# Kernel optimization log

Hardware: AMD Instinct MI355X
Metric: run time of the kernel (lower is better)

Reference implementation:

```python
import jax, jax.numpy as jnp
import numpy as np

N = 4096      # nodes
F = 512       # input_dim
D = 512       # output_dim
H = 8         # n_heads
d = D // H    # per-head out_sz


def setup_inputs() -> dict:
    key = jax.random.key(0)
    ks = jax.random.split(key, 6)
    x = jax.random.normal(ks[0], (N, F), dtype=jnp.float32)
    adj = (jax.random.uniform(ks[1], (N, N)) < 0.01).astype(jnp.float32)
    adj = jnp.maximum(adj, jnp.eye(N, dtype=jnp.float32))
    # per-head params: weight transform W, attention vectors a1/a2 (conv1d k=1 -> dot) with biases
    W = jax.random.normal(ks[2], (H, F, d), dtype=jnp.float32) * 0.05
    a1 = jax.random.normal(ks[3], (H, d), dtype=jnp.float32) * 0.05
    a2 = jax.random.normal(ks[4], (H, d), dtype=jnp.float32) * 0.05
    b1 = jnp.zeros((H,), dtype=jnp.float32)
    b2 = jnp.zeros((H,), dtype=jnp.float32)
    return {"x": x, "adj": adj, "W": W, "a1": a1, "b1": b1, "a2": a2, "b2": b2}


def reference(x, adj, W, a1, b1, a2, b2):
    # per-node linear transform for all heads: [H, N, d]
    seq_fts = jnp.einsum('nf,hfd->hnd', x, W)
    # attention logits components (conv1d(out=1,k=1) == dot + bias): [H, N]
    f1 = jnp.einsum('hnd,hd->hn', seq_fts, a1) + b1[:, None]
    f2 = jnp.einsum('hnd,hd->hn', seq_fts, a2) + b2[:, None]
    # logits = adj * f1_i + adj * f2_j  (adj acts multiplicatively AND as sparsity mask)
    logits = adj[None, :, :] * f1[:, :, None] + adj[None, :, :] * f2[:, None, :]
    lrelu = jnp.maximum(0.2 * logits, logits)  # leaky_relu alpha=0.2
    # sparse softmax over adjacency nonzeros (tf.sparse_softmax over from_dense pattern)
    mask = adj != 0
    scores = jnp.where(mask[None, :, :], lrelu, -jnp.inf)
    coefs = jax.nn.softmax(scores, axis=-1)           # [H, N, N], zero off-mask
    vals = jnp.einsum('hnm,hmd->hnd', coefs, seq_fts)  # sparse-dense matmul per head
    # concat heads on feature axis, batch dim of 1, elu activation
    h = jnp.transpose(vals, (1, 0, 2)).reshape(N, H * d)[None, :, :]
    return jax.nn.elu(h)
```

## Files before the change

### kernel.cpp

```cpp
#include <hip/hip_runtime.h>
#include <math.h>

#define N_NODES 4096
#define F_DIM   512
#define D_DIM   512
#define H_HEADS 8
#define HD      64
#define CAP     128

typedef __attribute__((ext_vector_type(8))) short short8;
typedef __attribute__((ext_vector_type(4))) float f32x4;

__device__ __forceinline__ unsigned short f2bf(float f) {
    unsigned int u = __builtin_bit_cast(unsigned int, f);
    return (unsigned short)((u + 0x7FFFu + ((u >> 16) & 1u)) >> 16);
}
__device__ __forceinline__ float bflo(unsigned int u) {
    return __builtin_bit_cast(float, u << 16);
}
__device__ __forceinline__ float bfhi(unsigned int u) {
    return __builtin_bit_cast(float, u & 0xffff0000u);
}

__global__ __launch_bounds__(256) void conv_w(const float* __restrict__ W,
                                              unsigned short* __restrict__ Bt) {
    const int t = blockIdx.x * 256 + threadIdx.x;
    const int n = t >> 6;
    const int kb = (t & 63) * 8;
    const int h = n >> 6, dd = n & 63;
    const float* src = W + (size_t)h * F_DIM * HD + dd;
    unsigned short o[8];
    #pragma unroll
    for (int q = 0; q < 8; ++q) o[q] = f2bf(src[(size_t)(kb + q) * HD]);
    *(uint4*)&Bt[(size_t)n * F_DIM + kb] = *(const uint4*)o;
}

__global__ __launch_bounds__(256) void mega(const float* __restrict__ x,
                                            const unsigned short* __restrict__ Bt,
                                            const float* __restrict__ adj,
                                            const float* __restrict__ a1,
                                            const float* __restrict__ b1,
                                            const float* __restrict__ a2,
                                            const float* __restrict__ b2,
                                            unsigned short* __restrict__ seqb,
                                            float* __restrict__ f1t,
                                            float* __restrict__ f2t,
                                            unsigned short* __restrict__ rowIdx,
                                            int* __restrict__ cntArr) {
    __shared__ unsigned short As[64][40];
    __shared__ unsigned short Bs[64][40];
    __shared__ float sF[2][64][2];

    const int tid  = threadIdx.x;
    const int lane = tid & 63;
    const int w    = tid >> 6;

    if (blockIdx.x >= 512) {
        const int r = (blockIdx.x - 512) * 4 + w;
        const float* arow = adj + (size_t)r * N_NODES;

        f32x4 vq[16];
        #pragma unroll
        for (int q = 0; q < 16; ++q)
            vq[q] = *(const f32x4*)&arow[q * 256 + lane * 4];

        unsigned long long mask = 0ull;
        #pragma unroll
        for (int q = 0; q < 16; ++q) {
            if (vq[q].x != 0.0f) mask |= 1ull << (q * 4 + 0);
            if (vq[q].y != 0.0f) mask |= 1ull << (q * 4 + 1);
            if (vq[q].z != 0.0f) mask |= 1ull << (q * 4 + 2);
            if (vq[q].w != 0.0f) mask |= 1ull << (q * 4 + 3);
        }
        const int n_t = __popcll(mask);
        int incl = n_t;
        #pragma unroll
        for (int off = 1; off < 64; off <<= 1) {
            int u = __shfl_up(incl, off, 64);
            if (lane >= off) incl += u;
        }
        const int tot = __shfl(incl, 63, 64);
        int pos = incl - n_t;
        unsigned short* rbase = rowIdx + (size_t)r * CAP;
        while (mask) {
            const int bit = __builtin_ctzll(mask);
            mask &= mask - 1;
            const int col = ((bit >> 2) << 8) + (lane << 2) + (bit & 3);
            if (pos < CAP)
                __builtin_nontemporal_store((unsigned short)col, rbase + pos);
            ++pos;
        }
        if (lane == 0) cntArr[r] = tot;
        return;
    }

    const int wr   = w >> 1, wc = w & 1;
    const int i0   = (blockIdx.x & 63) * 64;
    const int h    = blockIdx.x >> 6;
    const int n0   = h * 64;

    const int ar = tid >> 2;
    const int ac = (tid & 3) * 8;

    const int rlane = lane & 15;
    const int q     = lane >> 4;
    const int klane = q * 8;

    f32x4 acc[2][2] = {};

    for (int k0 = 0; k0 < F_DIM; k0 += 32) {
        const float* ga = &x[(size_t)(i0 + ar) * F_DIM + k0 + ac];
        const float4 xa = *(const float4*)ga;
        const float4 xb4 = *(const float4*)(ga + 4);
        unsigned short ao[8] = {f2bf(xa.x), f2bf(xa.y), f2bf(xa.z), f2bf(xa.w),
                                f2bf(xb4.x), f2bf(xb4.y), f2bf(xb4.z), f2bf(xb4.w)};
        const uint4 bv = *(const uint4*)&Bt[(size_t)(n0 + ar) * F_DIM + k0 + ac];
        __syncthreads();
        *(uint4*)&As[ar][ac] = *(const uint4*)ao;
        *(uint4*)&Bs[ar][ac] = bv;
        __syncthreads();

        short8 a_frag[2], b_frag[2];
        #pragma unroll
        for (int mi = 0; mi < 2; ++mi)
            a_frag[mi] = *(const short8*)&As[wr * 32 + mi * 16 + rlane][klane];
        #pragma unroll
        for (int ni = 0; ni < 2; ++ni)
            b_frag[ni] = *(const short8*)&Bs[wc * 32 + ni * 16 + rlane][klane];
        #pragma unroll
        for (int mi = 0; mi < 2; ++mi)
            #pragma unroll
            for (int ni = 0; ni < 2; ++ni)
                acc[mi][ni] = __builtin_amdgcn_mfma_f32_16x16x32_bf16(
                    a_frag[mi], b_frag[ni], acc[mi][ni], 0, 0, 0);
    }

    #pragma unroll
    for (int mi = 0; mi < 2; ++mi)
        #pragma unroll
        for (int ni = 0; ni < 2; ++ni)
            #pragma unroll
            for (int r = 0; r < 4; ++r) {
                const int row = i0 + wr * 32 + mi * 16 + q * 4 + r;
                const int col = n0 + wc * 32 + ni * 16 + rlane;
                seqb[(size_t)row * D_DIM + col] = f2bf(acc[mi][ni][r]);
            }

    float a1v[2], a2v[2];
    #pragma unroll
    for (int ni = 0; ni < 2; ++ni) {
        const int c = wc * 32 + ni * 16 + rlane;
        a1v[ni] = a1[h * HD + c];
        a2v[ni] = a2[h * HD + c];
    }
    #pragma unroll
    for (int mi = 0; mi < 2; ++mi)
        #pragma unroll
        for (int r = 0; r < 4; ++r) {
            float s1 = acc[mi][0][r] * a1v[0] + acc[mi][1][r] * a1v[1];
            float s2 = acc[mi][0][r] * a2v[0] + acc[mi][1][r] * a2v[1];
            #pragma unroll
            for (int m = 1; m < 16; m <<= 1) {
                s1 += __shfl_xor(s1, m, 64);
                s2 += __shfl_xor(s2, m, 64);
            }
            if (rlane == 0) {
                const int rl = wr * 32 + mi * 16 + q * 4 + r;
                sF[0][rl][wc] = s1;
                sF[1][rl][wc] = s2;
            }
        }
    __syncthreads();
    if (tid < 64) {
        const int row = i0 + tid;
        f1t[row * 8 + h] = sF[0][tid][0] + sF[0][tid][1] + b1[h];
        f2t[row * 8 + h] = sF[1][tid][0] + sF[1][tid][1] + b2[h];
    }
}

__global__ __launch_bounds__(128) void attn(const float* __restrict__ adj,
                                            const unsigned short* __restrict__ seqb,
                                            const float* __restrict__ f1t,
                                            const float* __restrict__ f2t,
                                            const unsigned short* __restrict__ rowIdx,
                                            const int* __restrict__ cntArr,
                                            float* __restrict__ out) {
    __shared__ int   sIdx[CAP];
    __shared__ float sP[CAP][8];
    __shared__ float sRedS[2][8];
    __shared__ float sAcc[64][8];

    const int i    = blockIdx.x;
    const int tid  = threadIdx.x;
    const int lane = tid & 63;
    const int w    = tid >> 6;
    const int h8   = lane >> 3;

    const int cnt = cntArr[i];

    const float4 f1a = *(const float4*)&f1t[i * 8];
    const float4 f1b = *(const float4*)&f1t[i * 8 + 4];
    const float f1r[8] = {f1a.x, f1a.y, f1a.z, f1a.w, f1b.x, f1b.y, f1b.z, f1b.w};

    float accv[8] = {0.f, 0.f, 0.f, 0.f, 0.f, 0.f, 0.f, 0.f};
    float myinv;

    if (cnt <= CAP) {
        int j = 0;
        float s[8] = {0.f, 0.f, 0.f, 0.f, 0.f, 0.f, 0.f, 0.f};
        float e[8] = {0.f, 0.f, 0.f, 0.f, 0.f, 0.f, 0.f, 0.f};
        if (tid < cnt) {
            j = (int)__builtin_nontemporal_load(rowIdx + (size_t)i * CAP + tid);
            const float4 fa = *(const float4*)&f2t[j * 8];
            const float4 fb = *(const float4*)&f2t[j * 8 + 4];
            const float f2r[8] = {fa.x, fa.y, fa.z, fa.w, fb.x, fb.y, fb.z, fb.w};
            #pragma unroll
            for (int h = 0; h < 8; ++h) {
                float v = f1r[h] + f2r[h];
                v = fmaxf(v, 0.2f * v);
                e[h] = __expf(v);
                s[h] = e[h];
            }
        }
        sIdx[tid] = j;
        f32x4 ea = {e[0], e[1], e[2], e[3]};
        f32x4 eb = {e[4], e[5], e[6], e[7]};
        *(f32x4*)&sP[tid][0] = ea;
        *(f32x4*)&sP[tid][4] = eb;

        #pragma unroll
        for (int off = 32; off; off >>= 1)
            #pragma unroll
            for (int h = 0; h < 8; ++h)
                s[h] += __shfl_xor(s[h], off, 64);
        if (lane == 0) {
            f32x4 sa = {s[0], s[1], s[2], s[3]};
            f32x4 sb = {s[4], s[5], s[6], s[7]};
            *(f32x4*)&sRedS[w][0] = sa;
            *(f32x4*)&sRedS[w][4] = sb;
        }
        __syncthreads();
        myinv = 1.0f / (sRedS[0][h8] + sRedS[1][h8]);

        const int G = (cnt + 3) >> 2;
        const char* __restrict__ vbase = (const char*)seqb + lane * 16;
        int g = w;
        if (g < G) {
            int4 jC = *(const int4*)&sIdx[g * 4];
            float pC0 = sP[g * 4 + 0][h8];
            float pC1 = sP[g * 4 + 1][h8];
            float pC2 = sP[g * 4 + 2][h8];
            float pC3 = sP[g * 4 + 3][h8];
            uint4 u0 = *(const uint4*)(vbase + ((size_t)jC.x << 10));
            uint4 u1 = *(const uint4*)(vbase + ((size_t)jC.y << 10));
            uint4 u2 = *(const uint4*)(vbase + ((size_t)jC.z << 10));
            uint4 u3 = *(const uint4*)(vbase + ((size_t)jC.w << 10));
            for (;;) {
                const int gn = g + 2;
                const bool more = gn < G;
                int4 jN;
                float pN0, pN1, pN2, pN3;
                uint4 v0, v1, v2, v3;
                if (more) {
                    jN = *(const int4*)&sIdx[gn * 4];
                    pN0 = sP[gn * 4 + 0][h8];
                    pN1 = sP[gn * 4 + 1][h8];
                    pN2 = sP[gn * 4 + 2][h8];
                    pN3 = sP[gn * 4 + 3][h8];
                    v0 = *(const uint4*)(vbase + ((size_t)jN.x << 10));
                    v1 = *(const uint4*)(vbase + ((size_t)jN.y << 10));
                    v2 = *(const uint4*)(vbase + ((size_t)jN.z << 10));
                    v3 = *(const uint4*)(vbase + ((size_t)jN.w << 10));
                }
                const unsigned int w0[4] = {u0.x, u0.y, u0.z, u0.w};
                const unsigned int w1[4] = {u1.x, u1.y, u1.z, u1.w};
                const unsigned int w2[4] = {u2.x, u2.y, u2.z, u2.w};
                const unsigned int w3[4] = {u3.x, u3.y, u3.z, u3.w};
                #pragma unroll
                for (int k = 0; k < 4; ++k) {
                    accv[k * 2 + 0] = fmaf(pC0, bflo(w0[k]), accv[k * 2 + 0]);
                    accv[k * 2 + 1] = fmaf(pC0, bfhi(w0[k]), accv[k * 2 + 1]);
                    accv[k * 2 + 0] = fmaf(pC1, bflo(w1[k]), accv[k * 2 + 0]);
                    accv[k * 2 + 1] = fmaf(pC1, bfhi(w1[k]), accv[k * 2 + 1]);
                    accv[k * 2 + 0] = fmaf(pC2, bflo(w2[k]), accv[k * 2 + 0]);
                    accv[k * 2 + 1] = fmaf(pC2, bfhi(w2[k]), accv[k * 2 + 1]);
                    accv[k * 2 + 0] = fmaf(pC3, bflo(w3[k]), accv[k * 2 + 0]);
                    accv[k * 2 + 1] = fmaf(pC3, bfhi(w3[k]), accv[k * 2 + 1]);
                }
                if (!more) break;
                u0 = v0; u1 = v1; u2 = v2; u3 = v3;
                pC0 = pN0; pC1 = pN1; pC2 = pN2; pC3 = pN3;
                g = gn;
            }
        }
    } else {
        const float* arow = adj + (size_t)i * N_NODES;
        float s[8] = {0.f, 0.f, 0.f, 0.f, 0.f, 0.f, 0.f, 0.f};
        for (int jx = tid; jx < N_NODES; jx += 128) {
            if (arow[jx] != 0.0f) {
                const float4 fa = *(const float4*)&f2t[jx * 8];
                const float4 fb = *(const float4*)&f2t[jx * 8 + 4];
                const float f2r[8] = {fa.x, fa.y, fa.z, fa.w, fb.x, fb.y, fb.z, fb.w};
                #pragma unroll
                for (int h = 0; h < 8; ++h) {
                    float v = f1r[h] + f2r[h];
                    v = fmaxf(v, 0.2f * v);
                    s[h] += __expf(v);
                }
            }
        }
        #pragma unroll
        for (int off = 32; off; off >>= 1)
            #pragma unroll
            for (int h = 0; h < 8; ++h)
                s[h] += __shfl_xor(s[h], off, 64);
        if (lane == 0) {
            f32x4 sa = {s[0], s[1], s[2], s[3]};
            f32x4 sb = {s[4], s[5], s[6], s[7]};
            *(f32x4*)&sRedS[w][0] = sa;
            *(f32x4*)&sRedS[w][4] = sb;
        }
        __syncthreads();
        myinv = 1.0f / (sRedS[0][h8] + sRedS[1][h8]);
        const float f1h = f1r[h8];

        const char* __restrict__ vbase = (const char*)seqb + lane * 16;
        const int jlo = w * (N_NODES / 2), jhi = jlo + N_NODES / 2;
        for (int jx = jlo; jx < jhi; ++jx) {
            if (arow[jx] != 0.0f) {
                float v = f1h + f2t[jx * 8 + h8];
                v = fmaxf(v, 0.2f * v);
                const float p = __expf(v);
                const uint4 u = *(const uint4*)(vbase + ((size_t)jx << 10));
                const unsigned int wv[4] = {u.x, u.y, u.z, u.w};
                #pragma unroll
                for (int k = 0; k < 4; ++k) {
                    accv[k * 2 + 0] = fmaf(p, bflo(wv[k]), accv[k * 2 + 0]);
                    accv[k * 2 + 1] = fmaf(p, bfhi(wv[k]), accv[k * 2 + 1]);
                }
            }
        }
    }

    if (w == 1) {
        f32x4 pa = {accv[0], accv[1], accv[2], accv[3]};
        f32x4 pb = {accv[4], accv[5], accv[6], accv[7]};
        *(f32x4*)&sAcc[lane][0] = pa;
        *(f32x4*)&sAcc[lane][4] = pb;
    }
    __syncthreads();
    if (w == 0) {
        float o[8];
        #pragma unroll
        for (int k = 0; k < 8; ++k) {
            const float v = (accv[k] + sAcc[lane][k]) * myinv;
            o[k] = (v > 0.f) ? v : expm1f(v);
        }
        f32x4 oa = {o[0], o[1], o[2], o[3]};
        f32x4 ob = {o[4], o[5], o[6], o[7]};
        float* dst = &out[(size_t)i * D_DIM + lane * 8];
        __builtin_nontemporal_store(oa, (f32x4*)dst);
        __builtin_nontemporal_store(ob, (f32x4*)(dst + 4));
    }
}

extern "C" void kernel_launch(void* const* d_in, const int* in_sizes, int n_in,
                              void* d_out, int out_size, void* d_ws, size_t ws_size,
                              hipStream_t stream) {
    const float* x   = (const float*)d_in[0];
    const float* adj = (const float*)d_in[1];
    const float* W   = (const float*)d_in[2];
    const float* a1  = (const float*)d_in[3];
    const float* b1  = (const float*)d_in[4];
    const float* a2  = (const float*)d_in[5];
    const float* b2  = (const float*)d_in[6];
    float* out = (float*)d_out;

    char* ws = (char*)d_ws;
    unsigned short* seqb = (unsigned short*)ws;
    unsigned short* Bt   = (unsigned short*)(ws + (size_t)N_NODES * D_DIM * 2);
    float* f1t = (float*)(ws + (size_t)N_NODES * D_DIM * 2 + (size_t)D_DIM * F_DIM * 2);
    float* f2t = f1t + (size_t)N_NODES * H_HEADS;
    unsigned short* rowIdx = (unsigned short*)(f2t + (size_t)N_NODES * H_HEADS);
    int* cntArr = (int*)(rowIdx + (size_t)N_NODES * CAP);

    conv_w<<<128, 256, 0, stream>>>(W, Bt);

    mega<<<1536, 256, 0, stream>>>(x, Bt, adj, a1, b1, a2, b2,
                                   seqb, f1t, f2t, rowIdx, cntArr);

    attn<<<N_NODES, 128, 0, stream>>>(adj, seqb, f1t, f2t, rowIdx, cntArr, out);
}
```

Baseline: 43.95 us.

## Split attention aggregation per row into two single-wave blocks by head half

The attention kernel now launches two 64-thread blocks per node, each handling four heads (half of the feature columns), instead of one 128-thread block that split neighbours across two waves. This removes the cross-wave softmax-sum and accumulator reductions through shared memory, so one wave keeps the whole softmax row. The trade-off is that each block recomputes the exp scores for its half, gathered loads shrink to 8 bytes per lane, and the software prefetch of the next neighbour group is gone.

```diff
diff --git a/kernel.cpp b/kernel.cpp
--- a/kernel.cpp
+++ b/kernel.cpp
@@ -178,131 +178,118 @@
     }
 }
 
-__global__ __launch_bounds__(128) void attn(const float* __restrict__ adj,
-                                            const unsigned short* __restrict__ seqb,
-                                            const float* __restrict__ f1t,
-                                            const float* __restrict__ f2t,
-                                            const unsigned short* __restrict__ rowIdx,
-                                            const int* __restrict__ cntArr,
-                                            float* __restrict__ out) {
+__global__ __launch_bounds__(64) void attn(const float* __restrict__ adj,
+                                           const unsigned short* __restrict__ seqb,
+                                           const float* __restrict__ f1t,
+                                           const float* __restrict__ f2t,
+                                           const unsigned short* __restrict__ rowIdx,
+                                           const int* __restrict__ cntArr,
+                                           float* __restrict__ out) {
     __shared__ int   sIdx[CAP];
-    __shared__ float sP[CAP][8];
-    __shared__ float sRedS[2][8];
-    __shared__ float sAcc[64][8];
-
-    const int i    = blockIdx.x;
-    const int tid  = threadIdx.x;
-    const int lane = tid & 63;
-    const int w    = tid >> 6;
-    const int h8   = lane >> 3;
+    __shared__ float sP[CAP][4];
+
+    const int bid  = blockIdx.x;
+    const int half = bid >> 12;
+    const int i    = bid & (N_NODES - 1);
+    const int lane = threadIdx.x;
+    const int hq   = lane >> 4;
 
     const int cnt = cntArr[i];
 
-    const float4 f1a = *(const float4*)&f1t[i * 8];
-    const float4 f1b = *(const float4*)&f1t[i * 8 + 4];
-    const float f1r[8] = {f1a.x, f1a.y, f1a.z, f1a.w, f1b.x, f1b.y, f1b.z, f1b.w};
-
-    float accv[8] = {0.f, 0.f, 0.f, 0.f, 0.f, 0.f, 0.f, 0.f};
+    const float4 f1h4 = *(const float4*)&f1t[i * 8 + half * 4];
+    const float f1r[4] = {f1h4.x, f1h4.y, f1h4.z, f1h4.w};
+
+    float accv[4] = {0.f, 0.f, 0.f, 0.f};
     float myinv;
 
     if (cnt <= CAP) {
-        int j = 0;
-        float s[8] = {0.f, 0.f, 0.f, 0.f, 0.f, 0.f, 0.f, 0.f};
-        float e[8] = {0.f, 0.f, 0.f, 0.f, 0.f, 0.f, 0.f, 0.f};
-        if (tid < cnt) {
-            j = (int)__builtin_nontemporal_load(rowIdx + (size_t)i * CAP + tid);
-            const float4 fa = *(const float4*)&f2t[j * 8];
-            const float4 fb = *(const float4*)&f2t[j * 8 + 4];
-            const float f2r[8] = {fa.x, fa.y, fa.z, fa.w, fb.x, fb.y, fb.z, fb.w};
-            #pragma unroll
-            for (int h = 0; h < 8; ++h) {
+        int j0 = 0, j1 = 0;
+        float e0[4] = {0.f, 0.f, 0.f, 0.f};
+        float e1[4] = {0.f, 0.f, 0.f, 0.f};
+        const bool has0 = lane < cnt;
+        const bool has1 = lane + 64 < cnt;
+        if (has0) {
+            j0 = (int)rowIdx[(size_t)i * CAP + lane];
+            const float4 fv = *(const float4*)&f2t[j0 * 8 + half * 4];
+            const float f2r[4] = {fv.x, fv.y, fv.z, fv.w};
+            #pragma unroll
+            for (int h = 0; h < 4; ++h) {
                 float v = f1r[h] + f2r[h];
                 v = fmaxf(v, 0.2f * v);
-                e[h] = __expf(v);
-                s[h] = e[h];
-            }
-        }
-        sIdx[tid] = j;
-        f32x4 ea = {e[0], e[1], e[2], e[3]};
-        f32x4 eb = {e[4], e[5], e[6], e[7]};
-        *(f32x4*)&sP[tid][0] = ea;
-        *(f32x4*)&sP[tid][4] = eb;
-
+                e0[h] = __expf(v);
+            }
+        }
+        if (has1) {
+            j1 = (int)rowIdx[(size_t)i * CAP + lane + 64];
+            const float4 fv = *(const float4*)&f2t[j1 * 8 + half * 4];
+            const float f2r[4] = {fv.x, fv.y, fv.z, fv.w};
+            #pragma unroll
+            for (int h = 0; h < 4; ++h) {
+                float v = f1r[h] + f2r[h];
+                v = fmaxf(v, 0.2f * v);
+                e1[h] = __expf(v);
+            }
+        }
+        sIdx[lane]      = j0;
+        sIdx[lane + 64] = j1;
+        f32x4 ea = {e0[0], e0[1], e0[2], e0[3]};
+        f32x4 eb = {e1[0], e1[1], e1[2], e1[3]};
+        *(f32x4*)&sP[lane][0]      = ea;
+        *(f32x4*)&sP[lane + 64][0] = eb;
+
+        float s[4];
+        #pragma unroll
+        for (int h = 0; h < 4; ++h) s[h] = e0[h] + e1[h];
         #pragma unroll
         for (int off = 32; off; off >>= 1)
             #pragma unroll
-            for (int h = 0; h < 8; ++h)
+            for (int h = 0; h < 4; ++h)
                 s[h] += __shfl_xor(s[h], off, 64);
-        if (lane == 0) {
-            f32x4 sa = {s[0], s[1], s[2], s[3]};
-            f32x4 sb = {s[4], s[5], s[6], s[7]};
-            *(f32x4*)&sRedS[w][0] = sa;
-            *(f32x4*)&sRedS[w][4] = sb;
-        }
+        myinv = 1.0f;
+        #pragma unroll
+        for (int h = 0; h < 4; ++h)
+            if (h == hq) myinv = 1.0f / s[h];
         __syncthreads();
-        myinv = 1.0f / (sRedS[0][h8] + sRedS[1][h8]);
-
+
+        const char* __restrict__ vbase =
+            (const char*)seqb + half * 512 + lane * 8;
         const int G = (cnt + 3) >> 2;
-        const char* __restrict__ vbase = (const char*)seqb + lane * 16;
-        int g = w;
-        if (g < G) {
-            int4 jC = *(const int4*)&sIdx[g * 4];
-            float pC0 = sP[g * 4 + 0][h8];
-            float pC1 = sP[g * 4 + 1][h8];
-            float pC2 = sP[g * 4 + 2][h8];
-            float pC3 = sP[g * 4 + 3][h8];
-            uint4 u0 = *(const uint4*)(vbase + ((size_t)jC.x << 10));
-            uint4 u1 = *(const uint4*)(vbase + ((size_t)jC.y << 10));
-            uint4 u2 = *(const uint4*)(vbase + ((size_t)jC.z << 10));
-            uint4 u3 = *(const uint4*)(vbase + ((size_t)jC.w << 10));
-            for (;;) {
-                const int gn = g + 2;
-                const bool more = gn < G;
-                int4 jN;
-                float pN0, pN1, pN2, pN3;
-                uint4 v0, v1, v2, v3;
-                if (more) {
-                    jN = *(const int4*)&sIdx[gn * 4];
-                    pN0 = sP[gn * 4 + 0][h8];
-                    pN1 = sP[gn * 4 + 1][h8];
-                    pN2 = sP[gn * 4 + 2][h8];
-                    pN3 = sP[gn * 4 + 3][h8];
-                    v0 = *(const uint4*)(vbase + ((size_t)jN.x << 10));
-                    v1 = *(const uint4*)(vbase + ((size_t)jN.y << 10));
-                    v2 = *(const uint4*)(vbase + ((size_t)jN.z << 10));
-                    v3 = *(const uint4*)(vbase + ((size_t)jN.w << 10));
-                }
-                const unsigned int w0[4] = {u0.x, u0.y, u0.z, u0.w};
-                const unsigned int w1[4] = {u1.x, u1.y, u1.z, u1.w};
-                const unsigned int w2[4] = {u2.x, u2.y, u2.z, u2.w};
-                const unsigned int w3[4] = {u3.x, u3.y, u3.z, u3.w};
-                #pragma unroll
-                for (int k = 0; k < 4; ++k) {
-                    accv[k * 2 + 0] = fmaf(pC0, bflo(w0[k]), accv[k * 2 + 0]);
-                    accv[k * 2 + 1] = fmaf(pC0, bfhi(w0[k]), accv[k * 2 + 1]);
-                    accv[k * 2 + 0] = fmaf(pC1, bflo(w1[k]), accv[k * 2 + 0]);
-                    accv[k * 2 + 1] = fmaf(pC1, bfhi(w1[k]), accv[k * 2 + 1]);
-                    accv[k * 2 + 0] = fmaf(pC2, bflo(w2[k]), accv[k * 2 + 0]);
-                    accv[k * 2 + 1] = fmaf(pC2, bfhi(w2[k]), accv[k * 2 + 1]);
-                    accv[k * 2 + 0] = fmaf(pC3, bflo(w3[k]), accv[k * 2 + 0]);
-                    accv[k * 2 + 1] = fmaf(pC3, bfhi(w3[k]), accv[k * 2 + 1]);
-                }
-                if (!more) break;
-                u0 = v0; u1 = v1; u2 = v2; u3 = v3;
-                pC0 = pN0; pC1 = pN1; pC2 = pN2; pC3 = pN3;
-                g = gn;
-            }
+        for (int g = 0; g < G; ++g) {
+            const int4  j4 = *(const int4*)&sIdx[g * 4];
+            const float p0 = sP[g * 4 + 0][hq];
+            const float p1 = sP[g * 4 + 1][hq];
+            const float p2 = sP[g * 4 + 2][hq];
+            const float p3 = sP[g * 4 + 3][hq];
+            const uint2 u0 = *(const uint2*)(vbase + ((size_t)j4.x << 10));
+            const uint2 u1 = *(const uint2*)(vbase + ((size_t)j4.y << 10));
+            const uint2 u2 = *(const uint2*)(vbase + ((size_t)j4.z << 10));
+            const uint2 u3 = *(const uint2*)(vbase + ((size_t)j4.w << 10));
+            accv[0] = fmaf(p0, bflo(u0.x), accv[0]);
+            accv[1] = fmaf(p0, bfhi(u0.x), accv[1]);
+            accv[2] = fmaf(p0, bflo(u0.y), accv[2]);
+            accv[3] = fmaf(p0, bfhi(u0.y), accv[3]);
+            accv[0] = fmaf(p1, bflo(u1.x), accv[0]);
+            accv[1] = fmaf(p1, bfhi(u1.x), accv[1]);
+            accv[2] = fmaf(p1, bflo(u1.y), accv[2]);
+            accv[3] = fmaf(p1, bfhi(u1.y), accv[3]);
+            accv[0] = fmaf(p2, bflo(u2.x), accv[0]);
+            accv[1] = fmaf(p2, bfhi(u2.x), accv[1]);
+            accv[2] = fmaf(p2, bflo(u2.y), accv[2]);
+            accv[3] = fmaf(p2, bfhi(u2.y), accv[3]);
+            accv[0] = fmaf(p3, bflo(u3.x), accv[0]);
+            accv[1] = fmaf(p3, bfhi(u3.x), accv[1]);
+            accv[2] = fmaf(p3, bflo(u3.y), accv[2]);
+            accv[3] = fmaf(p3, bfhi(u3.y), accv[3]);
         }
     } else {
         const float* arow = adj + (size_t)i * N_NODES;
-        float s[8] = {0.f, 0.f, 0.f, 0.f, 0.f, 0.f, 0.f, 0.f};
-        for (int jx = tid; jx < N_NODES; jx += 128) {
+        float s[4] = {0.f, 0.f, 0.f, 0.f};
+        for (int jx = lane; jx < N_NODES; jx += 64) {
             if (arow[jx] != 0.0f) {
-                const float4 fa = *(const float4*)&f2t[jx * 8];
-                const float4 fb = *(const float4*)&f2t[jx * 8 + 4];
-                const float f2r[8] = {fa.x, fa.y, fa.z, fa.w, fb.x, fb.y, fb.z, fb.w};
+                const float4 fv = *(const float4*)&f2t[jx * 8 + half * 4];
+                const float f2r[4] = {fv.x, fv.y, fv.z, fv.w};
                 #pragma unroll
-                for (int h = 0; h < 8; ++h) {
+                for (int h = 0; h < 4; ++h) {
                     float v = f1r[h] + f2r[h];
                     v = fmaxf(v, 0.2f * v);
                     s[h] += __expf(v);
@@ -312,56 +299,39 @@
         #pragma unroll
         for (int off = 32; off; off >>= 1)
             #pragma unroll
-            for (int h = 0; h < 8; ++h)
+            for (int h = 0; h < 4; ++h)
                 s[h] += __shfl_xor(s[h], off, 64);
-        if (lane == 0) {
-            f32x4 sa = {s[0], s[1], s[2], s[3]};
-            f32x4 sb = {s[4], s[5], s[6], s[7]};
-            *(f32x4*)&sRedS[w][0] = sa;
-            *(f32x4*)&sRedS[w][4] = sb;
-        }
-        __syncthreads();
-        myinv = 1.0f / (sRedS[0][h8] + sRedS[1][h8]);
-        const float f1h = f1r[h8];
-
-        const char* __restrict__ vbase = (const char*)seqb + lane * 16;
-        const int jlo = w * (N_NODES / 2), jhi = jlo + N_NODES / 2;
-        for (int jx = jlo; jx < jhi; ++jx) {
+        myinv = 1.0f;
+        #pragma unroll
+        for (int h = 0; h < 4; ++h)
+            if (h == hq) myinv = 1.0f / s[h];
+        const float f1h = f1r[hq];
+
+        const char* __restrict__ vbase =
+            (const char*)seqb + half * 512 + lane * 8;
+        for (int jx = 0; jx < N_NODES; ++jx) {
             if (arow[jx] != 0.0f) {
-                float v = f1h + f2t[jx * 8 + h8];
+                float v = f1h + f2t[jx * 8 + half * 4 + hq];
                 v = fmaxf(v, 0.2f * v);
                 const float p = __expf(v);
-                const uint4 u = *(const uint4*)(vbase + ((size_t)jx << 10));
-                const unsigned int wv[4] = {u.x, u.y, u.z, u.w};
-                #pragma unroll
-                for (int k = 0; k < 4; ++k) {
-                    accv[k * 2 + 0] = fmaf(p, bflo(wv[k]), accv[k * 2 + 0]);
-                    accv[k * 2 + 1] = fmaf(p, bfhi(wv[k]), accv[k * 2 + 1]);
-                }
-            }
-        }
-    }
-
-    if (w == 1) {
-        f32x4 pa = {accv[0], accv[1], accv[2], accv[3]};
-        f32x4 pb = {accv[4], accv[5], accv[6], accv[7]};
-        *(f32x4*)&sAcc[lane][0] = pa;
-        *(f32x4*)&sAcc[lane][4] = pb;
-    }
-    __syncthreads();
-    if (w == 0) {
-        float o[8];
-        #pragma unroll
-        for (int k = 0; k < 8; ++k) {
-            const float v = (accv[k] + sAcc[lane][k]) * myinv;
-            o[k] = (v > 0.f) ? v : expm1f(v);
-        }
-        f32x4 oa = {o[0], o[1], o[2], o[3]};
-        f32x4 ob = {o[4], o[5], o[6], o[7]};
-        float* dst = &out[(size_t)i * D_DIM + lane * 8];
-        __builtin_nontemporal_store(oa, (f32x4*)dst);
-        __builtin_nontemporal_store(ob, (f32x4*)(dst + 4));
-    }
+                const uint2 u = *(const uint2*)(vbase + ((size_t)jx << 10));
+                accv[0] = fmaf(p, bflo(u.x), accv[0]);
+                accv[1] = fmaf(p, bfhi(u.x), accv[1]);
+                accv[2] = fmaf(p, bflo(u.y), accv[2]);
+                accv[3] = fmaf(p, bfhi(u.y), accv[3]);
+            }
+        }
+    }
+
+    float o[4];
+    #pragma unroll
+    for (int k = 0; k < 4; ++k) {
+        const float v = accv[k] * myinv;
+        o[k] = (v > 0.f) ? v : expm1f(v);
+    }
+    f32x4 ov = {o[0], o[1], o[2], o[3]};
+    float* dst = &out[(size_t)i * D_DIM + half * 256 + lane * 4];
+    __builtin_nontemporal_store(ov, (f32x4*)dst);
 }
 
 extern "C" void kernel_launch(void* const* d_in, const int* in_sizes, int n_in,
@@ -389,5 +359,5 @@
     mega<<<1536, 256, 0, stream>>>(x, Bt, adj, a1, b1, a2, b2,
                                    seqb, f1t, f2t, rowIdx, cntArr);
 
-    attn<<<N_NODES, 128, 0, stream>>>(adj, seqb, f1t, f2t, rowIdx, cntArr, out);
-}
+    attn<<<2 * N_NODES, 64, 0, stream>>>(adj, seqb, f1t, f2t, rowIdx, cntArr, out);
+}
```

Result: no change. 44.78 us (+1.9%).
